# Kernel tuning notes

Hardware: AMD Instinct MI355X
Metric: run time of the kernel (lower is better)

## Reference

```python
import jax, jax.numpy as jnp
import numpy as np

B = 1; T = 2048; H = 2048; NH = 16; KVH = 4; HD = 128; WIN = 512; SINK = 64
S = 64; NG = 4; MLP_I = 5504; CK = 4
INTER = NH * HD; CONV_DIM = INTER + 2 * NG * S; NPROJ = INTER + CONV_DIM + NH
EPS = 1e-6; MEPS = 1e-5


def rmsnorm(x, w, eps):
    return x * jax.lax.rsqrt(jnp.mean(x * x, -1, keepdims=True) + eps) * w


def rotate_half(x):
    h = x.shape[-1] // 2
    return jnp.concatenate([-x[..., h:], x[..., :h]], -1)


def setup_inputs():
    key = jax.random.key(0)
    ks = jax.random.split(key, 32)
    rn = lambda k, s, sc=0.02: jax.random.normal(k, s, dtype=jnp.float32) * sc
    inv = 1.0 / (10000.0 ** (np.arange(0, HD, 2, dtype=np.float64) / HD))
    fr = np.outer(np.arange(T), inv)
    emb = np.concatenate([fr, fr], -1)
    return {
        'hidden_states': jax.random.normal(ks[0], (B, T, H), dtype=jnp.float32),
        'cos': jnp.asarray(np.cos(emb), jnp.float32)[None],
        'sin': jnp.asarray(np.sin(emb), jnp.float32)[None],
        'ln1_w': jnp.ones((H,), jnp.float32),
        'q_w': rn(ks[1], (NH * HD, H)), 'q_b': rn(ks[2], (NH * HD,)),
        'k_w': rn(ks[3], (KVH * HD, H)), 'k_b': rn(ks[4], (KVH * HD,)),
        'v_w': rn(ks[5], (KVH * HD, H)), 'v_b': rn(ks[6], (KVH * HD,)),
        'o_w': rn(ks[7], (H, NH * HD)),
        'in_proj_w': rn(ks[8], (NPROJ, H)),
        'conv_w': rn(ks[9], (CONV_DIM, 1, CK), 0.1),
        'conv_b': rn(ks[10], (CONV_DIM,), 0.1),
        'dt_bias': rn(ks[11], (NH,), 0.5),
        'A_log': rn(ks[12], (NH,), 0.5),
        'D': rn(ks[13], (NH,), 0.5),
        'mnorm_w': jnp.ones((INTER,), jnp.float32),
        'out_proj_w': rn(ks[14], (H, INTER)),
        'ln2_w': jnp.ones((H,), jnp.float32),
        'gate_w': rn(ks[15], (MLP_I, H)),
        'up_w': rn(ks[16], (MLP_I, H)),
        'down_w': rn(ks[17], (H, MLP_I)),
    }


def _mamba2(ev, in_proj_w, conv_w, conv_b, dt_bias, A_log, D, mnorm_w, out_proj_w):
    # ev: [B, L, H] evicted hidden states; Mamba2 with expand=1 (intermediate=INTER)
    L = ev.shape[1]
    proj = jnp.einsum('blh,ph->blp', ev, in_proj_w)
    z = proj[..., :INTER]
    xBC = proj[..., INTER:INTER + CONV_DIM]
    dt = proj[..., INTER + CONV_DIM:]
    # depthwise causal conv1d, kernel 4
    xBC = jax.lax.conv_general_dilated(
        xBC.transpose(0, 2, 1), conv_w, (1,), [(CK - 1, 0)],
        dimension_numbers=('NCH', 'OIH', 'NCH'), feature_group_count=CONV_DIM)
    xBC = jax.nn.silu((xBC + conv_b[None, :, None]).transpose(0, 2, 1))
    x = xBC[..., :INTER].reshape(B, L, NH, HD)
    Bm = jnp.repeat(xBC[..., INTER:INTER + NG * S].reshape(B, L, NG, S), NH // NG, axis=2)
    Cm = jnp.repeat(xBC[..., INTER + NG * S:].reshape(B, L, NG, S), NH // NG, axis=2)
    dt = jax.nn.softplus(dt + dt_bias)  # [B, L, NH]
    A = -jnp.exp(A_log)  # [NH]

    def scan_one(xb, bb, cb, db):
        def step(state, inp):
            xt, bt, ct, dtt = inp  # [NH,HD],[NH,S],[NH,S],[NH]
            decay = jnp.exp(dtt * A)[:, None, None]
            state = decay * state + (dtt[:, None] * xt)[..., None] * bt[:, None, :]
            y = jnp.einsum('hds,hs->hd', state, ct) + D[:, None] * xt
            return state, y
        _, ys = jax.lax.scan(step, jnp.zeros((NH, HD, S), xb.dtype), (xb, bb, cb, db))
        return ys

    y = jax.vmap(scan_one)(x, Bm, Cm, dt).reshape(B, L, INTER)
    g = y * jax.nn.silu(z)  # gated RMSNorm
    g = g * jax.lax.rsqrt(jnp.mean(g * g, -1, keepdims=True) + MEPS) * mnorm_w
    return jnp.einsum('bli,hi->blh', g, out_proj_w)


def reference(hidden_states, cos, sin, ln1_w, q_w, q_b, k_w, k_b, v_w, v_b, o_w,
              in_proj_w, conv_w, conv_b, dt_bias, A_log, D, mnorm_w, out_proj_w,
              ln2_w, gate_w, up_w, down_w):
    pre = rmsnorm(hidden_states, ln1_w, EPS)  # input_layernorm
    evict_end = T - WIN
    mem_out = _mamba2(pre[:, SINK:evict_end, :], in_proj_w, conv_w, conv_b,
                      dt_bias, A_log, D, mnorm_w, out_proj_w)  # [B, Le, H]
    mem_act = mem_out[:, -1:, :]

    def qkv(x, w, b, nh):
        return (jnp.einsum('blh,ph->blp', x, w) + b).reshape(x.shape[0], x.shape[1], nh, HD).transpose(0, 2, 1, 3)

    q = qkv(pre, q_w, q_b, NH)
    k = qkv(pre, k_w, k_b, KVH)
    v = qkv(pre, v_w, v_b, KVH)
    c = cos[:, None]; s = sin[:, None]
    q = q * c + rotate_half(q) * s
    k = k * c + rotate_half(k) * s
    # mem token injection at position SINK (mem projections are not rotated)
    q = q.at[:, :, SINK, :].set(qkv(mem_act, q_w, q_b, NH)[:, :, 0, :])
    k = k.at[:, :, SINK, :].set(qkv(mem_act, k_w, k_b, KVH)[:, :, 0, :])
    v = v.at[:, :, SINK, :].set(qkv(mem_act, v_w, v_b, KVH)[:, :, 0, :])
    # sink + sliding-window causal mask with mem-token bias
    row = jnp.arange(T)[:, None]; col = jnp.arange(T)[None, :]
    protected = SINK + 1
    bad = (col > row) | ((col < row - WIN) & (col >= protected))
    minv = jnp.finfo(jnp.float32).min
    mask = jnp.where(bad, minv, 0.0)[None, None]
    le_fact = (T - SINK - WIN) / T
    mask = mask.at[..., SINK].add(0.5 * le_fact)
    rep = NH // KVH
    kf = jnp.repeat(k, rep, axis=1)
    vf = jnp.repeat(v, rep, axis=1)
    scores = jnp.einsum('bhqd,bhkd->bhqk', q, kf) * (HD ** -0.5) + mask
    attn = jax.nn.softmax(scores, axis=-1)
    o = jnp.einsum('bhqk,bhkd->bhqd', attn, vf).transpose(0, 2, 1, 3).reshape(B, T, NH * HD)
    # training-path merge: sinks | mem_out | window
    merged = jnp.concatenate([o[:, :SINK], mem_out, o[:, T - WIN:]], axis=1)
    attn_out = jnp.einsum('blp,hp->blh', merged, o_w)
    h = hidden_states + attn_out
    m = rmsnorm(h, ln2_w, EPS)
    mlp = jnp.einsum('bli,hi->blh',
                     jax.nn.silu(jnp.einsum('blh,ih->bli', m, gate_w)) * jnp.einsum('blh,ih->bli', m, up_w),
                     down_w)
    return h + mlp
```

## Files before the change

kernel.cpp:

```cpp
#include <hip/hip_runtime.h>
#include <hip/hip_bf16.h>

#define TSEQ   2048
#define HDIM   2048
#define NHEAD  16
#define KVHEAD 4
#define HEADD  128
#define WINSZ  512
#define SINKN  64
#define MLPI   5504
#define CONVD  2560
#define NPROJD 4624
#define LMEM   1472
#define NCHUNK 23
#define QKVD   3072

typedef unsigned short bf_t;
typedef __attribute__((ext_vector_type(8))) short short8;
typedef __attribute__((ext_vector_type(4))) short s4v;
typedef __attribute__((ext_vector_type(4))) float ffrag;

#define BOF_PRE   0ull
#define BOF_QKV   8388608ull
#define BOF_P     8388608ull
#define BOF_S     20447232ull
#define BOF_PROJ  33554432ull
#define BOF_GB    33554432ull
#define BOF_XBCC  60780544ull
#define BOF_GF    75853824ull
#define BOF_MERG  75853824ull
#define BOF_GN    87912448ull
#define BOF_H     93941760ull
#define BOF_DT    110718976ull
#define BOF_GA    110813184ull
#define BOF_FLAG  110907392ull
#define BOF_LC    110908416ull

#define BOF_CNV_A 8388608ull
#define BOF_CNV_B 60780544ull

__device__ __forceinline__ float bf2f(bf_t x) { return __uint_as_float(((unsigned)x) << 16); }
__device__ __forceinline__ bf_t f2bf(float x) {
  unsigned u = __float_as_uint(x);
  return (bf_t)((u + 0x7FFFu + ((u >> 16) & 1u)) >> 16);
}
__device__ __forceinline__ float ldin(const void* p, size_t i, int bf) {
  if (bf) return bf2f(((const bf_t*)p)[i]);
  return ((const float*)p)[i];
}
__device__ __forceinline__ float siluf(float x) { return x / (1.f + expf(-x)); }

typedef const __attribute__((address_space(1))) unsigned gl_u32;
typedef __attribute__((address_space(3))) unsigned lds_u32;
__device__ __forceinline__ void gld16(const void* g, void* l) {
  __builtin_amdgcn_global_load_lds((gl_u32*)g, (lds_u32*)l, 16, 0, 0);
}

__global__ void detect_k(const void* __restrict__ ln1, int* __restrict__ flag) {
  unsigned w0 = *(const unsigned*)ln1;
  *flag = (w0 == 0x3F803F80u) ? 1 : 0;
}

__global__ __launch_bounds__(256) void wconv_k(const float* __restrict__ src,
    bf_t* __restrict__ dst, int n8, const int* __restrict__ flagp) {
  if (*flagp) return;
  int idx = blockIdx.x*256 + threadIdx.x;
  if (idx >= n8) return;
  const float* s = src + (size_t)idx*8;
  float4 a = *(const float4*)s, b = *(const float4*)(s+4);
  short8 o;
  o[0]=(short)f2bf(a.x); o[1]=(short)f2bf(a.y); o[2]=(short)f2bf(a.z); o[3]=(short)f2bf(a.w);
  o[4]=(short)f2bf(b.x); o[5]=(short)f2bf(b.y); o[6]=(short)f2bf(b.z); o[7]=(short)f2bf(b.w);
  *(short8*)(dst + (size_t)idx*8) = o;
}

__global__ __launch_bounds__(256) void rms_in_k(const void* __restrict__ x,
    const void* __restrict__ w, bf_t* __restrict__ out, float eps,
    const int* __restrict__ flagp) {
  int bf = *flagp;
  int row = blockIdx.x, tid = threadIdx.x;
  float v[8];
  if (bf) {
    const bf_t* xr = (const bf_t*)x + (size_t)row*HDIM + tid*8;
#pragma unroll
    for (int j = 0; j < 8; ++j) v[j] = bf2f(xr[j]);
  } else {
    const float* xr = (const float*)x + (size_t)row*HDIM + tid*8;
    float4 a = *(const float4*)xr, b = *(const float4*)(xr+4);
    v[0]=a.x; v[1]=a.y; v[2]=a.z; v[3]=a.w; v[4]=b.x; v[5]=b.y; v[6]=b.z; v[7]=b.w;
  }
  float ss = 0.f;
#pragma unroll
  for (int j = 0; j < 8; ++j) ss += v[j]*v[j];
  __shared__ float red[256];
  red[tid] = ss; __syncthreads();
  for (int s = 128; s > 0; s >>= 1) { if (tid < s) red[tid] += red[tid+s]; __syncthreads(); }
  float scale = 1.f / sqrtf(red[0]*(1.f/HDIM) + eps);
  bf_t* o = out + (size_t)row*HDIM + tid*8;
#pragma unroll
  for (int j = 0; j < 8; ++j) o[j] = f2bf(v[j]*scale*ldin(w, tid*8+j, bf));
}

__global__ __launch_bounds__(256) void rms_f2b_k(const float* __restrict__ x,
    const void* __restrict__ w, bf_t* __restrict__ out, float eps,
    const int* __restrict__ flagp) {
  int bf = *flagp;
  int row = blockIdx.x, tid = threadIdx.x;
  const float* xr = x + (size_t)row*2048 + tid*8;
  float4 a = *(const float4*)xr, b = *(const float4*)(xr+4);
  float v[8] = {a.x,a.y,a.z,a.w,b.x,b.y,b.z,b.w};
  float ss = 0.f;
#pragma unroll
  for (int j = 0; j < 8; ++j) ss += v[j]*v[j];
  __shared__ float red[256];
  red[tid] = ss; __syncthreads();
  for (int s = 128; s > 0; s >>= 1) { if (tid < s) red[tid] += red[tid+s]; __syncthreads(); }
  float scale = 1.f / sqrtf(red[0]*(1.f/2048.f) + eps);
  bf_t* o = out + (size_t)row*2048 + tid*8;
#pragma unroll
  for (int j = 0; j < 8; ++j) o[j] = f2bf(v[j]*scale*ldin(w, tid*8+j, bf));
}

__global__ __launch_bounds__(256) void tgemm_k(
    const bf_t* __restrict__ A, int lda,
    const void* __restrict__ W0, const void* __restrict__ W1, const void* __restrict__ W2,
    const bf_t* __restrict__ C0, const bf_t* __restrict__ C1, const bf_t* __restrict__ C2,
    int ldw, int n1, int n2,
    const void* __restrict__ b0, const void* __restrict__ b1, const void* __restrict__ b2,
    const void* __restrict__ res,
    const float* __restrict__ hf,
    void* __restrict__ out,
    int ldc, int M, int N, int K, int mode, int outbf,
    const int* __restrict__ flagp) {
  int bf = *flagp;
  __shared__ short As[8192];
  __shared__ short Bs[4096];
  int tid = threadIdx.x;
  int lane = tid & 63, wv = tid >> 6;
  int bm = blockIdx.y << 7, bn = blockIdx.x << 6;

  int trow = tid >> 2;
  int kc = (tid & 3) << 3;
  int ar0 = bm + trow;        if (ar0 > M-1) ar0 = M-1;
  int ar1 = bm + 64 + trow;   if (ar1 > M-1) ar1 = M-1;
  int wr  = bn + trow;        if (wr > N-1) wr = N-1;
  const bf_t* ga0 = A + (size_t)ar0*lda + kc;
  const bf_t* ga1 = A + (size_t)ar1*lda + kc;
  const bf_t* w0 = bf ? (const bf_t*)W0 : C0;
  const bf_t* w1 = bf ? (const bf_t*)W1 : C1;
  const bf_t* w2 = bf ? (const bf_t*)W2 : C2;
  const bf_t* Wsel; int wrl;
  if (wr < n1)      { Wsel = w0; wrl = wr; }
  else if (wr < n2) { Wsel = w1; wrl = wr - n1; }
  else              { Wsel = w2; wrl = wr - n2; }
  const bf_t* gwb = Wsel + (size_t)wrl*ldw + kc;
  int sA = wv*512;

  int wm = (wv & 1) << 6, wn = (wv >> 1) << 5;
  int fr = lane & 15, fq = (lane >> 4) << 3;

  ffrag acc[4][2];
#pragma unroll
  for (int i = 0; i < 4; ++i)
#pragma unroll
    for (int j = 0; j < 2; ++j) acc[i][j] = (ffrag){0.f,0.f,0.f,0.f};

  gld16(ga0, As + sA);
  gld16(ga1, As + 2048 + sA);
  gld16(gwb, Bs + sA);
  __syncthreads();

  int cur = 0;
  for (int k0 = 0; k0 < K; k0 += 32) {
    int nxt = k0 + 32;
    int nb = (cur ^ 1) << 12;
    int nbB = (cur ^ 1) << 11;
    if (nxt < K) {
      gld16(ga0 + nxt, As + nb + sA);
      gld16(ga1 + nxt, As + nb + 2048 + sA);
      gld16(gwb + nxt, Bs + nbB + sA);
    }
    int cbA = cur << 12, cbB = cur << 11;
    short8 af[4], bfr[2];
#pragma unroll
    for (int i = 0; i < 4; ++i)
      af[i] = *(const short8*)&As[cbA + (wm + i*16 + fr)*32 + fq];
#pragma unroll
    for (int j = 0; j < 2; ++j)
      bfr[j] = *(const short8*)&Bs[cbB + (wn + j*16 + fr)*32 + fq];
#pragma unroll
    for (int i = 0; i < 4; ++i)
#pragma unroll
      for (int j = 0; j < 2; ++j)
        acc[i][j] = __builtin_amdgcn_mfma_f32_16x16x32_bf16(af[i], bfr[j], acc[i][j], 0, 0, 0);
    __syncthreads();
    cur ^= 1;
  }

  int rbase = (lane >> 4) << 2;
  int cbase = lane & 15;
#pragma unroll
  for (int i = 0; i < 4; ++i) {
#pragma unroll
    for (int j = 0; j < 2; ++j) {
#pragma unroll
      for (int r = 0; r < 4; ++r) {
        int m = bm + wm + i*16 + rbase + r;
        int n = bn + wn + j*16 + cbase;
        if (m >= M || n >= N) continue;
        size_t ci = (size_t)m*ldc + n;
        float v = acc[i][j][r];
        if (mode == 0) {
          if (b0) {
            if (n < n1)      v += ldin(b0, n, bf);
            else if (n < n2) v += ldin(b1, n - n1, bf);
            else             v += ldin(b2, n - n2, bf);
          }
          if (outbf) ((bf_t*)out)[ci] = f2bf(v); else ((float*)out)[ci] = v;
        } else if (mode == 1) {
          ((float*)out)[ci] = v + ldin(res, ci, bf);
        } else {
          float hv = hf[ci] + v;
          if (bf) ((bf_t*)out)[ci] = f2bf(hv); else ((float*)out)[ci] = hv;
        }
      }
    }
  }
}

__global__ __launch_bounds__(256) void fgemm_k(
    const bf_t* __restrict__ A, int lda,
    const void* __restrict__ Wg, const void* __restrict__ Wu,
    const bf_t* __restrict__ Cg, const bf_t* __restrict__ Cu, int ldw,
    bf_t* __restrict__ out, int M, int N, int K,
    const int* __restrict__ flagp) {
  int bf = *flagp;
  __shared__ short As[8192];
  __shared__ short Bs[8192];
  int tid = threadIdx.x;
  int lane = tid & 63, wv = tid >> 6;
  int bm = blockIdx.y << 7, bn = blockIdx.x << 6;

  int trow = tid >> 2;
  int kc = (tid & 3) << 3;
  int ar0 = bm + trow;        if (ar0 > M-1) ar0 = M-1;
  int ar1 = bm + 64 + trow;   if (ar1 > M-1) ar1 = M-1;
  int wr  = bn + trow;        if (wr > N-1) wr = N-1;
  const bf_t* ga0 = A + (size_t)ar0*lda + kc;
  const bf_t* ga1 = A + (size_t)ar1*lda + kc;
  const bf_t* wg = bf ? (const bf_t*)Wg : Cg;
  const bf_t* wu = bf ? (const bf_t*)Wu : Cu;
  const bf_t* gwgb = wg + (size_t)wr*ldw + kc;
  const bf_t* gwub = wu + (size_t)wr*ldw + kc;
  int sA = wv*512;

  int wm = (wv & 1) << 6, wn = (wv >> 1) << 5;
  int fr = lane & 15, fq = (lane >> 4) << 3;

  ffrag ag[4][2], au[4][2];
#pragma unroll
  for (int i = 0; i < 4; ++i)
#pragma unroll
    for (int j = 0; j < 2; ++j) { ag[i][j] = (ffrag){0.f,0.f,0.f,0.f}; au[i][j] = (ffrag){0.f,0.f,0.f,0.f}; }

  gld16(ga0, As + sA);
  gld16(ga1, As + 2048 + sA);
  gld16(gwgb, Bs + sA);
  gld16(gwub, Bs + 2048 + sA);
  __syncthreads();

  int cur = 0;
  for (int k0 = 0; k0 < K; k0 += 32) {
    int nxt = k0 + 32;
    int nb = (cur ^ 1) << 12;
    if (nxt < K) {
      gld16(ga0 + nxt, As + nb + sA);
      gld16(ga1 + nxt, As + nb + 2048 + sA);
      gld16(gwgb + nxt, Bs + nb + sA);
      gld16(gwub + nxt, Bs + nb + 2048 + sA);
    }
    int cb = cur << 12;
    short8 af[4], bg[2], bu[2];
#pragma unroll
    for (int i = 0; i < 4; ++i)
      af[i] = *(const short8*)&As[cb + (wm + i*16 + fr)*32 + fq];
#pragma unroll
    for (int j = 0; j < 2; ++j) {
      bg[j] = *(const short8*)&Bs[cb + (wn + j*16 + fr)*32 + fq];
      bu[j] = *(const short8*)&Bs[cb + 2048 + (wn + j*16 + fr)*32 + fq];
    }
#pragma unroll
    for (int i = 0; i < 4; ++i)
#pragma unroll
      for (int j = 0; j < 2; ++j) {
        ag[i][j] = __builtin_amdgcn_mfma_f32_16x16x32_bf16(af[i], bg[j], ag[i][j], 0, 0, 0);
        au[i][j] = __builtin_amdgcn_mfma_f32_16x16x32_bf16(af[i], bu[j], au[i][j], 0, 0, 0);
      }
    __syncthreads();
    cur ^= 1;
  }

  int rbase = (lane >> 4) << 2;
  int cbase = lane & 15;
#pragma unroll
  for (int i = 0; i < 4; ++i)
#pragma unroll
    for (int j = 0; j < 2; ++j)
#pragma unroll
      for (int r = 0; r < 4; ++r) {
        int m = bm + wm + i*16 + rbase + r;
        int n = bn + wn + j*16 + cbase;
        if (m >= M || n >= N) continue;
        float g = ag[i][j][r], u = au[i][j][r];
        out[(size_t)m*N + n] = f2bf(siluf(g) * u);
      }
}

__global__ __launch_bounds__(256) void rope_k(float* __restrict__ tb, int stride,
    const void* __restrict__ cosp, const void* __restrict__ sinp,
    int nheads, const int* __restrict__ flagp) {
  int bf = *flagp;
  int idx = blockIdx.x*256 + threadIdx.x;
  int d = idx & 63;
  int rem = idx >> 6;
  int tpos = rem / nheads, hh = rem % nheads;
  float* base = tb + (size_t)tpos*stride + hh*128;
  float a = base[d], b = base[d+64];
  float c0 = ldin(cosp, (size_t)tpos*128 + d, bf),    s0 = ldin(sinp, (size_t)tpos*128 + d, bf);
  float c1 = ldin(cosp, (size_t)tpos*128 + d + 64, bf), s1 = ldin(sinp, (size_t)tpos*128 + d + 64, bf);
  base[d]    = a*c0 - b*s0;
  base[d+64] = b*c1 + a*s1;
}

__global__ __launch_bounds__(256) void conv_k(const float* __restrict__ proj,
    const void* __restrict__ convw, const void* __restrict__ convb,
    float* __restrict__ xbcc, const int* __restrict__ flagp) {
  int bf = *flagp;
  int idx = blockIdx.x*256 + threadIdx.x;
  int t = idx / CONVD, c = idx % CONVD;
  float acc = ldin(convb, c, bf);
#pragma unroll
  for (int j = 0; j < 4; ++j) {
    int tt = t - 3 + j;
    if (tt >= 0) acc += ldin(convw, (size_t)c*4 + j, bf) * proj[(size_t)tt*NPROJD + 2048 + c];
  }
  xbcc[idx] = siluf(acc);
}

__global__ __launch_bounds__(256) void dt_k(const float* __restrict__ proj,
    const void* __restrict__ dtb, const void* __restrict__ alog,
    float* __restrict__ dtv, float* __restrict__ ga, const int* __restrict__ flagp) {
  int bf = *flagp;
  int idx = blockIdx.x*256 + threadIdx.x;
  int t = idx >> 4, h = idx & 15;
  float raw = proj[(size_t)t*NPROJD + 4608 + h] + ldin(dtb, h, bf);
  float dt = (raw > 30.f) ? raw : log1pf(expf(raw));
  float A = -expf(ldin(alog, h, bf));
  dtv[idx] = dt;
  ga[idx] = dt*A;
}

__global__ __launch_bounds__(256) void cums_k(const float* __restrict__ ga,
    float* __restrict__ Lc) {
  int wid = blockIdx.x*4 + (threadIdx.x >> 6);
  int lane = threadIdx.x & 63;
  int h = wid / NCHUNK, c = wid % NCHUNK;
  int t = c*64 + lane;
  float a = ga[(size_t)t*16 + h];
#pragma unroll
  for (int off = 1; off < 64; off <<= 1) {
    float o = __shfl_up(a, off, 64);
    if (lane >= off) a += o;
  }
  Lc[(size_t)(h*NCHUNK + c)*64 + lane] = a;
}

__global__ __launch_bounds__(256) void chunkstate_k(
    const float* __restrict__ xbcc, const float* __restrict__ dtv,
    const float* __restrict__ Lc, float* __restrict__ Pbuf) {
  __shared__ short XT[128*72];
  __shared__ short BT[64*72];
  __shared__ float wj[64];
  int tid = threadIdx.x, lane = tid & 63, wv = tid >> 6;
  int b = blockIdx.x;
  int h = b & 15, c = b >> 4;
  int g64 = (h >> 2) << 6;
  size_t hc = (size_t)(h*NCHUNK + c);

  if (tid < 64) {
    float L63 = Lc[hc*64 + 63];
    float Lj  = Lc[hc*64 + tid];
    wj[tid] = dtv[(size_t)(c*64 + tid)*16 + h] * expf(L63 - Lj);
  }
  __syncthreads();
  for (int base = tid*4; base < 8192; base += 1024) {
    int j = base >> 7, d = base & 127;
    float4 xv = *(const float4*)&xbcc[(size_t)(c*64 + j)*CONVD + h*128 + d];
    XT[(d+0)*72 + j] = (short)f2bf(xv.x);
    XT[(d+1)*72 + j] = (short)f2bf(xv.y);
    XT[(d+2)*72 + j] = (short)f2bf(xv.z);
    XT[(d+3)*72 + j] = (short)f2bf(xv.w);
  }
  for (int base = tid*4; base < 4096; base += 1024) {
    int j = base >> 6, s = base & 63;
    float w = wj[j];
    float4 bv = *(const float4*)&xbcc[(size_t)(c*64 + j)*CONVD + 2048 + g64 + s];
    BT[(s+0)*72 + j] = (short)f2bf(bv.x * w);
    BT[(s+1)*72 + j] = (short)f2bf(bv.y * w);
    BT[(s+2)*72 + j] = (short)f2bf(bv.z * w);
    BT[(s+3)*72 + j] = (short)f2bf(bv.w * w);
  }
  __syncthreads();

  int fr = lane & 15, fq = (lane >> 4) << 3;
  ffrag acc[2][4];
#pragma unroll
  for (int i = 0; i < 2; ++i)
#pragma unroll
    for (int j = 0; j < 4; ++j) acc[i][j] = (ffrag){0.f,0.f,0.f,0.f};
#pragma unroll
  for (int k0 = 0; k0 < 64; k0 += 32) {
    short8 af[2], bfr[4];
#pragma unroll
    for (int i = 0; i < 2; ++i)
      af[i] = *(const short8*)&XT[(wv*32 + i*16 + fr)*72 + k0 + fq];
#pragma unroll
    for (int j = 0; j < 4; ++j)
      bfr[j] = *(const short8*)&BT[(j*16 + fr)*72 + k0 + fq];
#pragma unroll
    for (int i = 0; i < 2; ++i)
#pragma unroll
      for (int j = 0; j < 4; ++j)
        acc[i][j] = __builtin_amdgcn_mfma_f32_16x16x32_bf16(af[i], bfr[j], acc[i][j], 0, 0, 0);
  }
  int rbase = (lane >> 4) << 2, cbase = lane & 15;
#pragma unroll
  for (int i = 0; i < 2; ++i)
#pragma unroll
    for (int j = 0; j < 4; ++j)
#pragma unroll
      for (int r = 0; r < 4; ++r) {
        int d = wv*32 + i*16 + rbase + r;
        int s = j*16 + cbase;
        Pbuf[hc*8192 + d*64 + s] = acc[i][j][r];
      }
}

__global__ __launch_bounds__(256) void statepass_k(
    const float* __restrict__ Pbuf, const float* __restrict__ Lc,
    float* __restrict__ Sbuf) {
  int gid = blockIdx.x*256 + threadIdx.x;
  int h = gid >> 13, rem = gid & 8191;
  float s = 0.f;
  for (int c = 0; c < NCHUNK; ++c) {
    size_t hc = (size_t)(h*NCHUNK + c);
    Sbuf[hc*8192 + rem] = s;
    s = expf(Lc[hc*64 + 63]) * s + Pbuf[hc*8192 + rem];
  }
}

__global__ __launch_bounds__(256) void chunkout_k(
    const float* __restrict__ xbcc, const float* __restrict__ proj,
    const float* __restrict__ dtv, const float* __restrict__ Lc,
    const float* __restrict__ Sbuf, const void* __restrict__ Dp,
    float* __restrict__ g, const int* __restrict__ flagp) {
  __shared__ short Cs[64*72];
  __shared__ short BsS[64*72];
  __shared__ short XT[128*72];
  __shared__ short Sinb[128*72];
  __shared__ float Lch[64];
  __shared__ float dtch[64];
  int bf = *flagp;
  int tid = threadIdx.x, lane = tid & 63, wv = tid >> 6;
  int b = blockIdx.x;
  int h = b & 15, c = b >> 4;
  int g64 = (h >> 2) << 6;
  size_t hc = (size_t)(h*NCHUNK + c);
  float Dh = ldin(Dp, h, bf);

  if (tid < 64) {
    Lch[tid]  = Lc[hc*64 + tid];
    dtch[tid] = dtv[(size_t)(c*64 + tid)*16 + h];
  }
  for (int base = tid*4; base < 4096; base += 1024) {
    int i = base >> 6, s = base & 63;
    float4 cv = *(const float4*)&xbcc[(size_t)(c*64 + i)*CONVD + 2304 + g64 + s];
    Cs[i*72 + s+0] = (short)f2bf(cv.x); Cs[i*72 + s+1] = (short)f2bf(cv.y);
    Cs[i*72 + s+2] = (short)f2bf(cv.z); Cs[i*72 + s+3] = (short)f2bf(cv.w);
    float4 bv = *(const float4*)&xbcc[(size_t)(c*64 + i)*CONVD + 2048 + g64 + s];
    BsS[i*72 + s+0] = (short)f2bf(bv.x); BsS[i*72 + s+1] = (short)f2bf(bv.y);
    BsS[i*72 + s+2] = (short)f2bf(bv.z); BsS[i*72 + s+3] = (short)f2bf(bv.w);
  }
  for (int base = tid*4; base < 8192; base += 1024) {
    int j = base >> 7, d = base & 127;
    float4 xv = *(const float4*)&xbcc[(size_t)(c*64 + j)*CONVD + h*128 + d];
    XT[(d+0)*72 + j] = (short)f2bf(xv.x);
    XT[(d+1)*72 + j] = (short)f2bf(xv.y);
    XT[(d+2)*72 + j] = (short)f2bf(xv.z);
    XT[(d+3)*72 + j] = (short)f2bf(xv.w);
  }
  for (int base = tid*4; base < 8192; base += 1024) {
    int d = base >> 6, s = base & 63;
    float4 sv = *(const float4*)&Sbuf[hc*8192 + d*64 + s];
    Sinb[d*72 + s+0] = (short)f2bf(sv.x); Sinb[d*72 + s+1] = (short)f2bf(sv.y);
    Sinb[d*72 + s+2] = (short)f2bf(sv.z); Sinb[d*72 + s+3] = (short)f2bf(sv.w);
  }
  __syncthreads();

  int fr = lane & 15, fq = (lane >> 4) << 3;
  ffrag s0[4];
#pragma unroll
  for (int i = 0; i < 4; ++i) s0[i] = (ffrag){0.f,0.f,0.f,0.f};
#pragma unroll
  for (int k0 = 0; k0 < 64; k0 += 32) {
    short8 bfr = *(const short8*)&BsS[(wv*16 + fr)*72 + k0 + fq];
#pragma unroll
    for (int i = 0; i < 4; ++i) {
      short8 af = *(const short8*)&Cs[(i*16 + fr)*72 + k0 + fq];
      s0[i] = __builtin_amdgcn_mfma_f32_16x16x32_bf16(af, bfr, s0[i], 0, 0, 0);
    }
  }
  __syncthreads();

  {
    int rbase = (lane >> 4) << 2, cbase = lane & 15;
    int j = wv*16 + cbase;
#pragma unroll
    for (int i = 0; i < 4; ++i)
#pragma unroll
      for (int r = 0; r < 4; ++r) {
        int ii = i*16 + rbase + r;
        float v = (j <= ii) ? s0[i][r] * expf(Lch[ii] - Lch[j]) * dtch[j] : 0.f;
        BsS[ii*72 + j] = (short)f2bf(v);
      }
#pragma unroll
    for (int e = 0; e < 16; ++e) {
      int idx = tid*16 + e;
      int ii = idx >> 6, s = idx & 63;
      Cs[ii*72 + s] = (short)f2bf(bf2f((bf_t)Cs[ii*72 + s]) * expf(Lch[ii]));
    }
  }
  __syncthreads();

  ffrag acc[4][2];
#pragma unroll
  for (int i = 0; i < 4; ++i)
#pragma unroll
    for (int j = 0; j < 2; ++j) acc[i][j] = (ffrag){0.f,0.f,0.f,0.f};
#pragma unroll
  for (int k0 = 0; k0 < 64; k0 += 32) {
    short8 xb[2], af[4];
#pragma unroll
    for (int j = 0; j < 2; ++j)
      xb[j] = *(const short8*)&XT[(wv*32 + j*16 + fr)*72 + k0 + fq];
#pragma unroll
    for (int i = 0; i < 4; ++i)
      af[i] = *(const short8*)&BsS[(i*16 + fr)*72 + k0 + fq];
#pragma unroll
    for (int i = 0; i < 4; ++i)
#pragma unroll
      for (int j = 0; j < 2; ++j)
        acc[i][j] = __builtin_amdgcn_mfma_f32_16x16x32_bf16(af[i], xb[j], acc[i][j], 0, 0, 0);
  }
#pragma unroll
  for (int k0 = 0; k0 < 64; k0 += 32) {
    short8 sb[2], af[4];
#pragma unroll
    for (int j = 0; j < 2; ++j)
      sb[j] = *(const short8*)&Sinb[(wv*32 + j*16 + fr)*72 + k0 + fq];
#pragma unroll
    for (int i = 0; i < 4; ++i)
      af[i] = *(const short8*)&Cs[(i*16 + fr)*72 + k0 + fq];
#pragma unroll
    for (int i = 0; i < 4; ++i)
#pragma unroll
      for (int j = 0; j < 2; ++j)
        acc[i][j] = __builtin_amdgcn_mfma_f32_16x16x32_bf16(af[i], sb[j], acc[i][j], 0, 0, 0);
  }

  int rbase = (lane >> 4) << 2, cbase = lane & 15;
#pragma unroll
  for (int i = 0; i < 4; ++i)
#pragma unroll
    for (int j = 0; j < 2; ++j)
#pragma unroll
      for (int r = 0; r < 4; ++r) {
        int ii = i*16 + rbase + r;
        int d = wv*32 + j*16 + cbase;
        int t = c*64 + ii;
        int col = h*128 + d;
        float x = xbcc[(size_t)t*CONVD + col];
        float z = proj[(size_t)t*NPROJD + col];
        float y = acc[i][j][r] + Dh*x;
        g[(size_t)t*2048 + col] = y * siluf(z);
      }
}

__global__ __launch_bounds__(256) void memact_k(
    const bf_t* __restrict__ merged,
    const void* __restrict__ qw, const void* __restrict__ qb,
    const void* __restrict__ kw, const void* __restrict__ kb,
    const void* __restrict__ vw, const void* __restrict__ vb,
    const bf_t* __restrict__ cq, const bf_t* __restrict__ ck, const bf_t* __restrict__ cv,
    float* __restrict__ qkv, const int* __restrict__ flagp) {
  int bf = *flagp;
  int p = blockIdx.x, tid = threadIdx.x;
  const bf_t* ma = merged + (size_t)1535*2048;
  const void* b; const bf_t* wb; int off;
  if (p < 2048)      { wb = bf ? (const bf_t*)qw : cq; b = qb; off = p; }
  else if (p < 2560) { wb = bf ? (const bf_t*)kw : ck; b = kb; off = p - 2048; }
  else               { wb = bf ? (const bf_t*)vw : cv; b = vb; off = p - 2560; }
  float partial = 0.f;
  size_t wbase = (size_t)off*2048;
  for (int j = tid; j < 2048; j += 256) partial += bf2f(ma[j])*bf2f(wb[wbase + j]);
  __shared__ float red[256];
  red[tid] = partial; __syncthreads();
  for (int s = 128; s > 0; s >>= 1) { if (tid < s) red[tid] += red[tid+s]; __syncthreads(); }
  if (tid == 0) qkv[(size_t)64*QKVD + p] = red[0] + ldin(b, off, bf);
}

__global__ __launch_bounds__(256) void attn3_k(
    const float* __restrict__ qkv, bf_t* __restrict__ merged) {
  __shared__ short Qs[64*136];
  __shared__ short Ks[64*136];
  __shared__ short Vt[128*72];
  __shared__ short Pb[64*72];

  int bid = blockIdx.x;
  int g = bid & 3, hg = (bid >> 2) & 3, qt = bid >> 4;
  int r0 = (qt == 0) ? 0 : (1536 + 64*(qt-1));
  int tid = threadIdx.x, lane = tid & 63, wv = tid >> 6;

  int qcol = g*512 + hg*128;
  int kcol = 2048 + g*128;
  int vcol = 2560 + g*128;

  int fr = lane & 15, fq = (lane >> 4) << 3;
  int rloc = (lane >> 4) << 2;
  int cb = lane & 15;

  {
    int row = tid >> 2, c4 = tid & 3;
    const float* qp = qkv + (size_t)(r0 + row)*QKVD + qcol;
#pragma unroll
    for (int rep = 0; rep < 8; ++rep) {
      int d = (c4 + rep*4)*4;
      float4 v = *(const float4*)(qp + d);
      s4v o;
      o[0] = (short)f2bf(v.x); o[1] = (short)f2bf(v.y);
      o[2] = (short)f2bf(v.z); o[3] = (short)f2bf(v.w);
      *(s4v*)&Qs[row*136 + d] = o;
    }
  }
  __syncthreads();

  float m4[4] = {-3.0e38f, -3.0e38f, -3.0e38f, -3.0e38f};
  float l4[4] = {0.f, 0.f, 0.f, 0.f};
  ffrag o8[8];
#pragma unroll
  for (int n = 0; n < 8; ++n) o8[n] = (ffrag){0.f,0.f,0.f,0.f};

  int ntiles = (qt == 0) ? 1 : 11;
  for (int t = 0; t < ntiles; ++t) {
    int kb = (t == 0) ? 0 : ((t == 1) ? 64 : (r0 - 512 + 64*(t-2)));

    {
      int row = tid >> 2, c4 = tid & 3;
      const float* kp = qkv + (size_t)(kb + row)*QKVD + kcol;
#pragma unroll
      for (int rep = 0; rep < 8; ++rep) {
        int d = (c4 + rep*4)*4;
        float4 v = *(const float4*)(kp + d);
        s4v o;
        o[0] = (short)f2bf(v.x); o[1] = (short)f2bf(v.y);
        o[2] = (short)f2bf(v.z); o[3] = (short)f2bf(v.w);
        *(s4v*)&Ks[row*136 + d] = o;
      }
    }
#pragma unroll
    for (int it = 0; it < 8; ++it) {
      int task = tid + it*256;
      int d = task & 127, jg = task >> 7;
      const float* vp = qkv + (size_t)(kb + jg*4)*QKVD + vcol + d;
      s4v o;
      o[0] = (short)f2bf(vp[0]);
      o[1] = (short)f2bf(vp[QKVD]);
      o[2] = (short)f2bf(vp[2*QKVD]);
      o[3] = (short)f2bf(vp[3*QKVD]);
      *(s4v*)&Vt[d*72 + jg*4] = o;
    }
    __syncthreads();

    ffrag s[4];
#pragma unroll
    for (int n = 0; n < 4; ++n) s[n] = (ffrag){0.f,0.f,0.f,0.f};
#pragma unroll
    for (int k0 = 0; k0 < 128; k0 += 32) {
      short8 aq = *(const short8*)&Qs[(wv*16 + fr)*136 + k0 + fq];
#pragma unroll
      for (int n = 0; n < 4; ++n) {
        short8 bk = *(const short8*)&Ks[(n*16 + fr)*136 + k0 + fq];
        s[n] = __builtin_amdgcn_mfma_f32_16x16x32_bf16(aq, bk, s[n], 0, 0, 0);
      }
    }

    float tmax[4] = {-INFINITY, -INFINITY, -INFINITY, -INFINITY};
#pragma unroll
    for (int n = 0; n < 4; ++n) {
      int kk = kb + n*16 + cb;
      float bias = (kk == 64) ? 0.359375f : 0.f;
#pragma unroll
      for (int rg = 0; rg < 4; ++rg) {
        int rr = r0 + wv*16 + rloc + rg;
        bool ok = (kk <= rr) && ((kk >= rr - 512) || (kk < 65));
        float sv = ok ? (s[n][rg]*0.08838834764831845f + bias) : -INFINITY;
        s[n][rg] = sv;
        tmax[rg] = fmaxf(tmax[rg], sv);
      }
    }
    float sc4[4];
#pragma unroll
    for (int rg = 0; rg < 4; ++rg) {
#pragma unroll
      for (int off = 1; off < 16; off <<= 1)
        tmax[rg] = fmaxf(tmax[rg], __shfl_xor(tmax[rg], off, 64));
      float mnew = fmaxf(m4[rg], tmax[rg]);
      sc4[rg] = expf(m4[rg] - mnew);
      m4[rg] = mnew;
      l4[rg] *= sc4[rg];
    }
#pragma unroll
    for (int n = 0; n < 8; ++n)
#pragma unroll
      for (int rg = 0; rg < 4; ++rg) o8[n][rg] *= sc4[rg];

    float ts[4] = {0.f, 0.f, 0.f, 0.f};
#pragma unroll
    for (int n = 0; n < 4; ++n)
#pragma unroll
      for (int rg = 0; rg < 4; ++rg) {
        float p = expf(s[n][rg] - m4[rg]);
        ts[rg] += p;
        Pb[(wv*16 + rloc + rg)*72 + n*16 + cb] = (short)f2bf(p);
      }
#pragma unroll
    for (int rg = 0; rg < 4; ++rg) {
#pragma unroll
      for (int off = 1; off < 16; off <<= 1) ts[rg] += __shfl_xor(ts[rg], off, 64);
      l4[rg] += ts[rg];
    }

#pragma unroll
    for (int k0 = 0; k0 < 64; k0 += 32) {
      short8 ap = *(const short8*)&Pb[(wv*16 + fr)*72 + k0 + fq];
#pragma unroll
      for (int n = 0; n < 8; ++n) {
        short8 bv = *(const short8*)&Vt[(n*16 + fr)*72 + k0 + fq];
        o8[n] = __builtin_amdgcn_mfma_f32_16x16x32_bf16(ap, bv, o8[n], 0, 0, 0);
      }
    }
    __syncthreads();
  }

  float inv[4];
#pragma unroll
  for (int rg = 0; rg < 4; ++rg) inv[rg] = 1.f / l4[rg];
#pragma unroll
  for (int n = 0; n < 8; ++n)
#pragma unroll
    for (int rg = 0; rg < 4; ++rg) {
      int i = wv*16 + rloc + rg;
      int d = n*16 + cb;
      merged[(size_t)(r0 + i)*2048 + (g*4 + hg)*128 + d] = f2bf(o8[n][rg]*inv[rg]);
    }
}

extern "C" void kernel_launch(void* const* d_in, const int* in_sizes, int n_in,
                              void* d_out, int out_size, void* d_ws, size_t ws_size,
                              hipStream_t stream) {
  const void* hidden = d_in[0];
  const void* cosp   = d_in[1];
  const void* sinp   = d_in[2];
  const void* ln1w   = d_in[3];
  const void* qw = d_in[4];  const void* qb = d_in[5];
  const void* kw = d_in[6];  const void* kb = d_in[7];
  const void* vw = d_in[8];  const void* vb = d_in[9];
  const void* ow = d_in[10];
  const void* inpw = d_in[11];
  const void* convw = d_in[12]; const void* convb = d_in[13];
  const void* dtb = d_in[14]; const void* alog = d_in[15]; const void* dd = d_in[16];
  const void* mnw = d_in[17]; const void* outpw = d_in[18];
  const void* ln2w = d_in[19];
  const void* gatew = d_in[20]; const void* upw = d_in[21]; const void* downw = d_in[22];

  char* wsb = (char*)d_ws;
  bf_t*  pre    = (bf_t*)(wsb + BOF_PRE);
  bf_t*  mbuf   = (bf_t*)(wsb + BOF_PRE);
  float* qkv    = (float*)(wsb + BOF_QKV);
  float* Pbuf   = (float*)(wsb + BOF_P);
  float* Sbuf   = (float*)(wsb + BOF_S);
  float* proj   = (float*)(wsb + BOF_PROJ);
  bf_t*  Gbuf   = (bf_t*)(wsb + BOF_GB);
  float* xbcc   = (float*)(wsb + BOF_XBCC);
  float* gbuf   = (float*)(wsb + BOF_GF);
  bf_t*  merged = (bf_t*)(wsb + BOF_MERG);
  bf_t*  gn     = (bf_t*)(wsb + BOF_GN);
  float* hbuf   = (float*)(wsb + BOF_H);
  float* dtv    = (float*)(wsb + BOF_DT);
  float* ga     = (float*)(wsb + BOF_GA);
  int*   flag   = (int*)(wsb + BOF_FLAG);
  float* Lc     = (float*)(wsb + BOF_LC);
  bf_t*  cvA    = (bf_t*)(wsb + BOF_CNV_A);
  bf_t*  cvB    = (bf_t*)(wsb + BOF_CNV_B);
  bf_t*  cvq    = cvB;
  bf_t*  cvk    = cvB + 4194304;
  bf_t*  cvv    = cvB + 5242880;

  detect_k<<<dim3(1), dim3(1), 0, stream>>>(ln1w, flag);
  rms_in_k<<<dim3(TSEQ), dim3(256), 0, stream>>>(hidden, ln1w, pre, 1e-6f, flag);

  wconv_k<<<dim3(4624), dim3(256), 0, stream>>>((const float*)inpw, cvA, 1183744, flag);
  tgemm_k<<<dim3(73,12), dim3(256), 0, stream>>>(pre + (size_t)64*2048, 2048,
      inpw, nullptr, nullptr, cvA, nullptr, nullptr, 2048, NPROJD, NPROJD,
      nullptr, nullptr, nullptr,
      nullptr, nullptr, proj, NPROJD, LMEM, NPROJD, 2048, 0, 0, flag);
  conv_k<<<dim3((LMEM*CONVD)/256), dim3(256), 0, stream>>>(proj, convw, convb, xbcc, flag);
  dt_k<<<dim3((LMEM*16)/256), dim3(256), 0, stream>>>(proj, dtb, alog, dtv, ga, flag);
  cums_k<<<dim3(92), dim3(256), 0, stream>>>(ga, Lc);
  chunkstate_k<<<dim3(368), dim3(256), 0, stream>>>(xbcc, dtv, Lc, Pbuf);
  statepass_k<<<dim3(512), dim3(256), 0, stream>>>(Pbuf, Lc, Sbuf);
  wconv_k<<<dim3(2048), dim3(256), 0, stream>>>((const float*)outpw, cvA, 524288, flag);
  chunkout_k<<<dim3(368), dim3(256), 0, stream>>>(xbcc, proj, dtv, Lc, Sbuf, dd, gbuf, flag);
  rms_f2b_k<<<dim3(LMEM), dim3(256), 0, stream>>>(gbuf, mnw, gn, 1e-5f, flag);
  tgemm_k<<<dim3(32,12), dim3(256), 0, stream>>>(gn, 2048,
      outpw, nullptr, nullptr, cvA, nullptr, nullptr, 2048, 2048, 2048,
      nullptr, nullptr, nullptr,
      nullptr, nullptr, merged + (size_t)64*2048, 2048, LMEM, 2048, 2048, 0, 1, flag);

  wconv_k<<<dim3(2048), dim3(256), 0, stream>>>((const float*)qw, cvq, 524288, flag);
  wconv_k<<<dim3(512),  dim3(256), 0, stream>>>((const float*)kw, cvk, 131072, flag);
  wconv_k<<<dim3(512),  dim3(256), 0, stream>>>((const float*)vw, cvv, 131072, flag);
  tgemm_k<<<dim3(48,16), dim3(256), 0, stream>>>(pre, 2048,
      qw, kw, vw, cvq, cvk, cvv, 2048, 2048, 2560, qb, kb, vb,
      nullptr, nullptr, qkv, QKVD, 2048, QKVD, 2048, 0, 0, flag);
  rope_k<<<dim3(8192), dim3(256), 0, stream>>>(qkv, QKVD, cosp, sinp, 16, flag);
  rope_k<<<dim3(2048), dim3(256), 0, stream>>>(qkv + 2048, QKVD, cosp, sinp, 4, flag);

  memact_k<<<dim3(3072), dim3(256), 0, stream>>>(merged, qw, qb, kw, kb, vw, vb,
      cvq, cvk, cvv, qkv, flag);
  attn3_k<<<dim3(144), dim3(256), 0, stream>>>(qkv, merged);

  wconv_k<<<dim3(2048), dim3(256), 0, stream>>>((const float*)ow, cvB, 524288, flag);
  tgemm_k<<<dim3(32,16), dim3(256), 0, stream>>>(merged, 2048,
      ow, nullptr, nullptr, cvB, nullptr, nullptr, 2048, 2048, 2048,
      nullptr, nullptr, nullptr,
      hidden, nullptr, hbuf, 2048, 2048, 2048, 2048, 1, 0, flag);
  rms_f2b_k<<<dim3(TSEQ), dim3(256), 0, stream>>>(hbuf, ln2w, mbuf, 1e-6f, flag);

  wconv_k<<<dim3(5504), dim3(256), 0, stream>>>((const float*)gatew, cvA, 1409024, flag);
  wconv_k<<<dim3(5504), dim3(256), 0, stream>>>((const float*)upw,   cvB, 1409024, flag);
  fgemm_k<<<dim3(86,16), dim3(256), 0, stream>>>(mbuf, 2048, gatew, upw, cvA, cvB, 2048,
      Gbuf, 2048, MLPI, 2048, flag);
  wconv_k<<<dim3(5504), dim3(256), 0, stream>>>((const float*)downw, cvA, 1409024, flag);
  tgemm_k<<<dim3(32,16), dim3(256), 0, stream>>>(Gbuf, MLPI,
      downw, nullptr, nullptr, cvA, nullptr, nullptr, MLPI, 2048, 2048,
      nullptr, nullptr, nullptr,
      nullptr, hbuf, d_out, 2048, 2048, 2048, MLPI, 3, 0, flag);
}
```

Before: 669.3 us.

## Swizzle LDS k-chunks and widen fused gate/up GEMM tile to 128x128

An XOR swizzle on the k-chunk offset is applied to both the global-to-LDS load layout and the fragment reads in tgemm_k and fgemm_k, to cut LDS bank conflicts. The fused gate/up GEMM tile grows from 128x64 to 128x128 with separate gate and up LDS buffers, 4x4 accumulator tiles per warp and launch_bounds(256,2), halving the grid. This raises reuse of the A tile but doubles accumulator registers and LDS per block, which may lower occupancy. The bounds clamp on weight rows was dropped; 5504 = 43*128, so rows stay in range.

```diff
diff --git a/kernel.cpp b/kernel.cpp
--- a/kernel.cpp
+++ b/kernel.cpp
@@ -140,7 +140,7 @@
   int bm = blockIdx.y << 7, bn = blockIdx.x << 6;
 
   int trow = tid >> 2;
-  int kc = (tid & 3) << 3;
+  int kc = (((tid & 3) ^ ((tid >> 3) & 3)) << 3);
   int ar0 = bm + trow;        if (ar0 > M-1) ar0 = M-1;
   int ar1 = bm + 64 + trow;   if (ar1 > M-1) ar1 = M-1;
   int wr  = bn + trow;        if (wr > N-1) wr = N-1;
@@ -157,7 +157,8 @@
   int sA = wv*512;
 
   int wm = (wv & 1) << 6, wn = (wv >> 1) << 5;
-  int fr = lane & 15, fq = (lane >> 4) << 3;
+  int fr = lane & 15;
+  int fq = (((lane >> 4) ^ ((fr >> 1) & 3)) << 3);
 
   ffrag acc[4][2];
 #pragma unroll
@@ -228,7 +229,7 @@
   }
 }
 
-__global__ __launch_bounds__(256) void fgemm_k(
+__global__ __launch_bounds__(256, 2) void fgemm_k(
     const bf_t* __restrict__ A, int lda,
     const void* __restrict__ Wg, const void* __restrict__ Wu,
     const bf_t* __restrict__ Cg, const bf_t* __restrict__ Cu, int ldw,
@@ -236,37 +237,42 @@
     const int* __restrict__ flagp) {
   int bf = *flagp;
   __shared__ short As[8192];
-  __shared__ short Bs[8192];
+  __shared__ short Bg[8192];
+  __shared__ short Bu[8192];
   int tid = threadIdx.x;
   int lane = tid & 63, wv = tid >> 6;
-  int bm = blockIdx.y << 7, bn = blockIdx.x << 6;
+  int bm = blockIdx.y << 7, bn = blockIdx.x << 7;
 
   int trow = tid >> 2;
-  int kc = (tid & 3) << 3;
+  int kc = (((tid & 3) ^ ((tid >> 3) & 3)) << 3);
   int ar0 = bm + trow;        if (ar0 > M-1) ar0 = M-1;
   int ar1 = bm + 64 + trow;   if (ar1 > M-1) ar1 = M-1;
-  int wr  = bn + trow;        if (wr > N-1) wr = N-1;
   const bf_t* ga0 = A + (size_t)ar0*lda + kc;
   const bf_t* ga1 = A + (size_t)ar1*lda + kc;
   const bf_t* wg = bf ? (const bf_t*)Wg : Cg;
   const bf_t* wu = bf ? (const bf_t*)Wu : Cu;
-  const bf_t* gwgb = wg + (size_t)wr*ldw + kc;
-  const bf_t* gwub = wu + (size_t)wr*ldw + kc;
+  const bf_t* gg0 = wg + (size_t)(bn + trow)*ldw + kc;
+  const bf_t* gg1 = wg + (size_t)(bn + 64 + trow)*ldw + kc;
+  const bf_t* gu0 = wu + (size_t)(bn + trow)*ldw + kc;
+  const bf_t* gu1 = wu + (size_t)(bn + 64 + trow)*ldw + kc;
   int sA = wv*512;
 
-  int wm = (wv & 1) << 6, wn = (wv >> 1) << 5;
-  int fr = lane & 15, fq = (lane >> 4) << 3;
-
-  ffrag ag[4][2], au[4][2];
+  int wm = (wv & 1) << 6, wn = (wv >> 1) << 6;
+  int fr = lane & 15;
+  int fq = (((lane >> 4) ^ ((fr >> 1) & 3)) << 3);
+
+  ffrag ag[4][4], au[4][4];
 #pragma unroll
   for (int i = 0; i < 4; ++i)
 #pragma unroll
-    for (int j = 0; j < 2; ++j) { ag[i][j] = (ffrag){0.f,0.f,0.f,0.f}; au[i][j] = (ffrag){0.f,0.f,0.f,0.f}; }
+    for (int j = 0; j < 4; ++j) { ag[i][j] = (ffrag){0.f,0.f,0.f,0.f}; au[i][j] = (ffrag){0.f,0.f,0.f,0.f}; }
 
   gld16(ga0, As + sA);
   gld16(ga1, As + 2048 + sA);
-  gld16(gwgb, Bs + sA);
-  gld16(gwub, Bs + 2048 + sA);
+  gld16(gg0, Bg + sA);
+  gld16(gg1, Bg + 2048 + sA);
+  gld16(gu0, Bu + sA);
+  gld16(gu1, Bu + 2048 + sA);
   __syncthreads();
 
   int cur = 0;
@@ -276,25 +282,27 @@
     if (nxt < K) {
       gld16(ga0 + nxt, As + nb + sA);
       gld16(ga1 + nxt, As + nb + 2048 + sA);
-      gld16(gwgb + nxt, Bs + nb + sA);
-      gld16(gwub + nxt, Bs + nb + 2048 + sA);
+      gld16(gg0 + nxt, Bg + nb + sA);
+      gld16(gg1 + nxt, Bg + nb + 2048 + sA);
+      gld16(gu0 + nxt, Bu + nb + sA);
+      gld16(gu1 + nxt, Bu + nb + 2048 + sA);
     }
     int cb = cur << 12;
-    short8 af[4], bg[2], bu[2];
+    short8 af[4], bgf[4], buf2[4];
 #pragma unroll
     for (int i = 0; i < 4; ++i)
       af[i] = *(const short8*)&As[cb + (wm + i*16 + fr)*32 + fq];
 #pragma unroll
-    for (int j = 0; j < 2; ++j) {
-      bg[j] = *(const short8*)&Bs[cb + (wn + j*16 + fr)*32 + fq];
-      bu[j] = *(const short8*)&Bs[cb + 2048 + (wn + j*16 + fr)*32 + fq];
+    for (int j = 0; j < 4; ++j) {
+      bgf[j]  = *(const short8*)&Bg[cb + (wn + j*16 + fr)*32 + fq];
+      buf2[j] = *(const short8*)&Bu[cb + (wn + j*16 + fr)*32 + fq];
     }
 #pragma unroll
     for (int i = 0; i < 4; ++i)
 #pragma unroll
-      for (int j = 0; j < 2; ++j) {
-        ag[i][j] = __builtin_amdgcn_mfma_f32_16x16x32_bf16(af[i], bg[j], ag[i][j], 0, 0, 0);
-        au[i][j] = __builtin_amdgcn_mfma_f32_16x16x32_bf16(af[i], bu[j], au[i][j], 0, 0, 0);
+      for (int j = 0; j < 4; ++j) {
+        ag[i][j] = __builtin_amdgcn_mfma_f32_16x16x32_bf16(af[i], bgf[j],  ag[i][j], 0, 0, 0);
+        au[i][j] = __builtin_amdgcn_mfma_f32_16x16x32_bf16(af[i], buf2[j], au[i][j], 0, 0, 0);
       }
     __syncthreads();
     cur ^= 1;
@@ -305,7 +313,7 @@
 #pragma unroll
   for (int i = 0; i < 4; ++i)
 #pragma unroll
-    for (int j = 0; j < 2; ++j)
+    for (int j = 0; j < 4; ++j)
 #pragma unroll
       for (int r = 0; r < 4; ++r) {
         int m = bm + wm + i*16 + rbase + r;
@@ -859,7 +867,7 @@
 
   wconv_k<<<dim3(5504), dim3(256), 0, stream>>>((const float*)gatew, cvA, 1409024, flag);
   wconv_k<<<dim3(5504), dim3(256), 0, stream>>>((const float*)upw,   cvB, 1409024, flag);
-  fgemm_k<<<dim3(86,16), dim3(256), 0, stream>>>(mbuf, 2048, gatew, upw, cvA, cvB, 2048,
+  fgemm_k<<<dim3(43,16), dim3(256), 0, stream>>>(mbuf, 2048, gatew, upw, cvA, cvB, 2048,
       Gbuf, 2048, MLPI, 2048, flag);
   wconv_k<<<dim3(5504), dim3(256), 0, stream>>>((const float*)downw, cvA, 1409024, flag);
   tgemm_k<<<dim3(32,16), dim3(256), 0, stream>>>(Gbuf, MLPI,
```

Result: no change. 676.0 us (+1.0%).
